# Kernel tuning notes

Measured on AMD Instinct MI355X. Metric: run time of the kernel, lower is better.

Reference implementation:

```python
import jax, jax.numpy as jnp
import numpy as np

NEG_SLOPE = 0.2  # PyG GATConv default negative_slope
EPS = 1e-16


def gat_conv(x, src, dst, num_nodes, W, att_src, att_dst, bias, concat):
    """PyG-style GATConv (eval mode, no dropout). att_*: [H, C]."""
    H, C = att_src.shape
    h = (x @ W).reshape(num_nodes, H, C)                      # [N,H,C]
    a_s = jnp.einsum('nhc,hc->nh', h, att_src)                # [N,H]
    a_d = jnp.einsum('nhc,hc->nh', h, att_dst)                # [N,H]
    e = jax.nn.leaky_relu(a_s[src] + a_d[dst], NEG_SLOPE)     # [E,H]
    # segment softmax over edges grouped by destination node
    m = jax.lax.stop_gradient(jax.ops.segment_max(e, dst, num_segments=num_nodes))
    ex = jnp.exp(e - m[dst])
    denom = jax.ops.segment_sum(ex, dst, num_segments=num_nodes)
    alpha = ex / (denom[dst] + EPS)                           # [E,H]
    msg = h[src] * alpha[:, :, None]                          # [E,H,C]
    out = jax.ops.segment_sum(msg, dst, num_segments=num_nodes)  # [N,H,C]
    out = out.reshape(num_nodes, H * C) if concat else out.mean(axis=1)
    return out + bias


def setup_inputs() -> dict:
    key = jax.random.key(0)
    ks = jax.random.split(key, 12)
    N, E = 65536, 1310720
    IN, HID, OUT, HEADS = 768, 128, 2, 8
    C1 = HID // HEADS  # 16
    s = 0.05
    return {
        'x': jax.random.normal(ks[0], (N, IN), jnp.float32),
        'edge_index': jax.random.randint(ks[1], (2, E), 0, N, jnp.int64),
        'W1': jax.random.normal(ks[2], (IN, HEADS * C1), jnp.float32) * s,
        'att_src1': jax.random.normal(ks[3], (HEADS, C1), jnp.float32) * s,
        'att_dst1': jax.random.normal(ks[4], (HEADS, C1), jnp.float32) * s,
        'b1': jnp.zeros((HID,), jnp.float32),
        'Wp': jax.random.normal(ks[5], (IN, HID), jnp.float32) * s,
        'bp': jnp.zeros((HID,), jnp.float32),
        'W2': jax.random.normal(ks[6], (HID, OUT), jnp.float32) * s,
        'att_src2': jax.random.normal(ks[7], (1, OUT), jnp.float32) * s,
        'att_dst2': jax.random.normal(ks[8], (1, OUT), jnp.float32) * s,
        'b2': jnp.zeros((OUT,), jnp.float32),
    }


def reference(x, edge_index, W1, att_src1, att_dst1, b1, Wp, bp, W2, att_src2, att_dst2, b2):
    N = x.shape[0]
    loops = jnp.arange(N, dtype=edge_index.dtype)  # add_self_loops=True
    src = jnp.concatenate([edge_index[0], loops])
    dst = jnp.concatenate([edge_index[1], loops])
    # eval mode: dropout is identity
    h1 = gat_conv(x, src, dst, N, W1, att_src1, att_dst1, b1, concat=True)
    h = jax.nn.elu(h1 + x @ Wp + bp)  # residual projection + ELU
    return gat_conv(h, src, dst, N, W2, att_src2, att_dst2, b2, concat=False)
```

## Files before the change

kernel.cpp:

```cpp
#include <hip/hip_runtime.h>
#include <hip/hip_bf16.h>
#include <math.h>

#define NEG_SLOPE 0.2f

typedef __attribute__((ext_vector_type(8))) short short8;
typedef __attribute__((ext_vector_type(4))) float float4v;

__device__ __forceinline__ unsigned f2bf(float f) {
  unsigned u = __builtin_bit_cast(unsigned, f);
  return (u + 0x7fffu + ((u >> 16) & 1u)) >> 16;
}
__device__ __forceinline__ float bflo(unsigned u) {
  return __builtin_bit_cast(float, u << 16);
}
__device__ __forceinline__ float bfhi(unsigned u) {
  return __builtin_bit_cast(float, u & 0xffff0000u);
}

__global__ __launch_bounds__(256) void convert_w(const float* __restrict__ W1,
                                                 const float* __restrict__ Wp,
                                                 short* __restrict__ Wt) {
  int k = blockIdx.x;
  int c = threadIdx.x;
  float v = (c < 128) ? W1[k * 128 + c] : Wp[k * 128 + (c - 128)];
  Wt[(size_t)c * 768 + k] = (short)f2bf(v);
}

__global__ __launch_bounds__(256) void gemm_mfma(const float* __restrict__ x,
                                                 const short* __restrict__ Wt,
                                                 float* __restrict__ proj,
                                                 unsigned* __restrict__ h1bf) {
  __shared__ short As[64][40];
  __shared__ short Bs[256][40];
  const int tid = threadIdx.x;
  const int wave = tid >> 6, lane = tid & 63;
  const int l15 = lane & 15, l4 = lane >> 4;
  const int row0 = blockIdx.x * 64;

  const int ar = tid >> 3;
  const int ak = (tid & 7) * 4;
  const int bc = tid >> 2;
  const int bk = (tid & 3) * 8;

  float4v acc[4][4] = {};

  for (int k0 = 0; k0 < 768; k0 += 32) {
#pragma unroll
    for (int i = 0; i < 2; i++) {
      int r = i * 32 + ar;
      float4 f = *(const float4*)&x[(size_t)(row0 + r) * 768 + k0 + ak];
      uint2 p;
      p.x = f2bf(f.x) | (f2bf(f.y) << 16);
      p.y = f2bf(f.z) | (f2bf(f.w) << 16);
      *(uint2*)&As[r][ak] = p;
    }
#pragma unroll
    for (int i = 0; i < 4; i++) {
      int c = i * 64 + bc;
      uint4 v = *(const uint4*)&Wt[(size_t)c * 768 + k0 + bk];
      *(uint4*)&Bs[c][bk] = v;
    }
    __syncthreads();

    short8 afr[4];
#pragma unroll
    for (int rt = 0; rt < 4; rt++)
      afr[rt] = *(const short8*)&As[rt * 16 + l15][l4 * 8];
#pragma unroll
    for (int ct = 0; ct < 4; ct++) {
      short8 bfr = *(const short8*)&Bs[wave * 64 + ct * 16 + l15][l4 * 8];
#pragma unroll
      for (int rt = 0; rt < 4; rt++)
        acc[rt][ct] =
            __builtin_amdgcn_mfma_f32_16x16x32_bf16(afr[rt], bfr, acc[rt][ct], 0, 0, 0);
    }
    __syncthreads();
  }

  const int colbase = wave * 64;
  if (wave < 2) {
#pragma unroll
    for (int ct = 0; ct < 4; ct++) {
      const int c = colbase + ct * 16 + l15;
#pragma unroll
      for (int rt = 0; rt < 4; rt++) {
#pragma unroll
        for (int r = 0; r < 4; r++) {
          const int R = row0 + rt * 16 + l4 * 4 + r;
          unsigned u = f2bf(acc[rt][ct][r]);
          unsigned up = __shfl_xor(u, 1);
          if ((l15 & 1) == 0) h1bf[(size_t)R * 64 + (c >> 1)] = u | (up << 16);
        }
      }
    }
  } else {
#pragma unroll
    for (int ct = 0; ct < 4; ct++) {
      const int c = colbase - 128 + ct * 16 + l15;
#pragma unroll
      for (int rt = 0; rt < 4; rt++) {
#pragma unroll
        for (int r = 0; r < 4; r++) {
          const int R = row0 + rt * 16 + l4 * 4 + r;
          proj[(size_t)R * 128 + c] = acc[rt][ct][r];
        }
      }
    }
  }
}

__global__ __launch_bounds__(256) void attn1b(const uint4* __restrict__ h1bf4,
                                              const float* __restrict__ att_src1,
                                              const float* __restrict__ att_dst1,
                                              float* __restrict__ a_s1,
                                              float* __restrict__ a_d1) {
  const int t = blockIdx.x * 256 + threadIdx.x;
  const int n = t >> 3, h = t & 7;
  uint4 q0 = h1bf4[(size_t)n * 16 + h * 2];
  uint4 q1 = h1bf4[(size_t)n * 16 + h * 2 + 1];
  float v[16];
  v[0] = bflo(q0.x); v[1] = bfhi(q0.x); v[2] = bflo(q0.y); v[3] = bfhi(q0.y);
  v[4] = bflo(q0.z); v[5] = bfhi(q0.z); v[6] = bflo(q0.w); v[7] = bfhi(q0.w);
  v[8] = bflo(q1.x); v[9] = bfhi(q1.x); v[10] = bflo(q1.y); v[11] = bfhi(q1.y);
  v[12] = bflo(q1.z); v[13] = bfhi(q1.z); v[14] = bflo(q1.w); v[15] = bfhi(q1.w);
  float as = 0.f, ad = 0.f;
#pragma unroll
  for (int i = 0; i < 16; i++) {
    as += v[i] * att_src1[h * 16 + i];
    ad += v[i] * att_dst1[h * 16 + i];
  }
  a_s1[t] = as;
  a_d1[t] = ad;
}

__global__ void init_counts(int* counts, int N) {
  int i = blockIdx.x * blockDim.x + threadIdx.x;
  if (i < N) counts[i] = 1;
}

__global__ void hist_kernel(const int* __restrict__ dst, int* counts, int E) {
  int i = blockIdx.x * blockDim.x + threadIdx.x;
  int base = i * 4;
  if (base + 3 < E) {
    int4 d = *(const int4*)&dst[base];
    atomicAdd(&counts[d.x], 1);
    atomicAdd(&counts[d.y], 1);
    atomicAdd(&counts[d.z], 1);
    atomicAdd(&counts[d.w], 1);
  } else {
    for (int j = base; j < E; j++) atomicAdd(&counts[dst[j]], 1);
  }
}

__global__ __launch_bounds__(256) void scan_a(const int* __restrict__ counts,
                                              int* offsets, int* bsum) {
  __shared__ int s[256];
  int t = threadIdx.x, idx = blockIdx.x * 256 + t;
  int v = counts[idx];
  s[t] = v;
  __syncthreads();
  for (int d = 1; d < 256; d <<= 1) {
    int x = (t >= d) ? s[t - d] : 0;
    __syncthreads();
    s[t] += x;
    __syncthreads();
  }
  offsets[idx] = s[t] - v;
  if (t == 255) bsum[blockIdx.x] = s[t];
}

__global__ __launch_bounds__(256) void scan_b(int* bsum) {
  __shared__ int s[256];
  int t = threadIdx.x;
  int v = bsum[t];
  s[t] = v;
  __syncthreads();
  for (int d = 1; d < 256; d <<= 1) {
    int x = (t >= d) ? s[t - d] : 0;
    __syncthreads();
    s[t] += x;
    __syncthreads();
  }
  bsum[t] = s[t] - v;
}

__global__ __launch_bounds__(256) void scan_c(int* offsets, const int* bsum,
                                              int* cursor, int* sortedsrc,
                                              int N, int Etot) {
  int t = threadIdx.x, idx = blockIdx.x * 256 + t;
  int off = offsets[idx] + bsum[blockIdx.x];
  offsets[idx] = off;
  sortedsrc[off] = idx;
  cursor[idx] = off + 1;
  if (idx == 0) offsets[N] = Etot;
}

__global__ void scatter_edges(const int* __restrict__ src,
                              const int* __restrict__ dst, int* cursor,
                              int* sortedsrc, int E) {
  int i = blockIdx.x * blockDim.x + threadIdx.x;
  int base = i * 4;
  if (base + 3 < E) {
    int4 s = *(const int4*)&src[base];
    int4 d = *(const int4*)&dst[base];
    sortedsrc[atomicAdd(&cursor[d.x], 1)] = s.x;
    sortedsrc[atomicAdd(&cursor[d.y], 1)] = s.y;
    sortedsrc[atomicAdd(&cursor[d.z], 1)] = s.z;
    sortedsrc[atomicAdd(&cursor[d.w], 1)] = s.w;
  } else {
    for (int j = base; j < E; j++)
      sortedsrc[atomicAdd(&cursor[dst[j]], 1)] = src[j];
  }
}

__global__ __launch_bounds__(256) void agg1_fused(
    const uint4* __restrict__ h1bf4, const float* __restrict__ proj,
    const float* __restrict__ a_s1, const float* __restrict__ a_d1,
    const int* __restrict__ offsets, const int* __restrict__ sortedsrc,
    const float* __restrict__ b1, const float* __restrict__ bp,
    const float* __restrict__ W2, const float* __restrict__ att_s2,
    const float* __restrict__ att_d2, float* __restrict__ h2,
    float* __restrict__ as2, float* __restrict__ ad2) {
  const int t = threadIdx.x;
  const int n = blockIdx.x * 16 + (t >> 4);
  const int k = t & 15;
  const int hd = k >> 1;
  const float ad = a_d1[n * 8 + hd];
  const int begin = offsets[n], end = offsets[n + 1];
  float acc[8] = {};
  float aw = 0.f;
  int j = begin;
  for (; j + 4 <= end; j += 4) {
    int s0 = sortedsrc[j], s1 = sortedsrc[j + 1];
    int s2 = sortedsrc[j + 2], s3 = sortedsrc[j + 3];
    float e0 = a_s1[s0 * 8 + hd], e1 = a_s1[s1 * 8 + hd];
    float e2 = a_s1[s2 * 8 + hd], e3 = a_s1[s3 * 8 + hd];
    uint4 q0 = h1bf4[(size_t)s0 * 16 + k];
    uint4 q1 = h1bf4[(size_t)s1 * 16 + k];
    uint4 q2 = h1bf4[(size_t)s2 * 16 + k];
    uint4 q3 = h1bf4[(size_t)s3 * 16 + k];
    e0 += ad; e1 += ad; e2 += ad; e3 += ad;
    float w0 = __expf(e0 > 0.f ? e0 : NEG_SLOPE * e0);
    float w1 = __expf(e1 > 0.f ? e1 : NEG_SLOPE * e1);
    float w2 = __expf(e2 > 0.f ? e2 : NEG_SLOPE * e2);
    float w3 = __expf(e3 > 0.f ? e3 : NEG_SLOPE * e3);
    acc[0] += w0 * bflo(q0.x) + w1 * bflo(q1.x) + w2 * bflo(q2.x) + w3 * bflo(q3.x);
    acc[1] += w0 * bfhi(q0.x) + w1 * bfhi(q1.x) + w2 * bfhi(q2.x) + w3 * bfhi(q3.x);
    acc[2] += w0 * bflo(q0.y) + w1 * bflo(q1.y) + w2 * bflo(q2.y) + w3 * bflo(q3.y);
    acc[3] += w0 * bfhi(q0.y) + w1 * bfhi(q1.y) + w2 * bfhi(q2.y) + w3 * bfhi(q3.y);
    acc[4] += w0 * bflo(q0.z) + w1 * bflo(q1.z) + w2 * bflo(q2.z) + w3 * bflo(q3.z);
    acc[5] += w0 * bfhi(q0.z) + w1 * bfhi(q1.z) + w2 * bfhi(q2.z) + w3 * bfhi(q3.z);
    acc[6] += w0 * bflo(q0.w) + w1 * bflo(q1.w) + w2 * bflo(q2.w) + w3 * bflo(q3.w);
    acc[7] += w0 * bfhi(q0.w) + w1 * bfhi(q1.w) + w2 * bfhi(q2.w) + w3 * bfhi(q3.w);
    aw += (w0 + w1) + (w2 + w3);
  }
  for (; j < end; j++) {
    int s0 = sortedsrc[j];
    float e0 = a_s1[s0 * 8 + hd] + ad;
    uint4 q0 = h1bf4[(size_t)s0 * 16 + k];
    float w0 = __expf(e0 > 0.f ? e0 : NEG_SLOPE * e0);
    acc[0] += w0 * bflo(q0.x);
    acc[1] += w0 * bfhi(q0.x);
    acc[2] += w0 * bflo(q0.y);
    acc[3] += w0 * bfhi(q0.y);
    acc[4] += w0 * bflo(q0.z);
    acc[5] += w0 * bfhi(q0.z);
    acc[6] += w0 * bflo(q0.w);
    acc[7] += w0 * bfhi(q0.w);
    aw += w0;
  }
  const float inv = 1.f / (aw + 1e-16f);
  const float4 pj0 = *(const float4*)&proj[(size_t)n * 128 + k * 8];
  const float4 pj1 = *(const float4*)&proj[(size_t)n * 128 + k * 8 + 4];
  const float4 b1a = *(const float4*)&b1[k * 8];
  const float4 b1b = *(const float4*)&b1[k * 8 + 4];
  const float4 bpa = *(const float4*)&bp[k * 8];
  const float4 bpb = *(const float4*)&bp[k * 8 + 4];
  float v[8];
  v[0] = acc[0] * inv + pj0.x + b1a.x + bpa.x;
  v[1] = acc[1] * inv + pj0.y + b1a.y + bpa.y;
  v[2] = acc[2] * inv + pj0.z + b1a.z + bpa.z;
  v[3] = acc[3] * inv + pj0.w + b1a.w + bpa.w;
  v[4] = acc[4] * inv + pj1.x + b1b.x + bpb.x;
  v[5] = acc[5] * inv + pj1.y + b1b.y + bpb.y;
  v[6] = acc[6] * inv + pj1.z + b1b.z + bpb.z;
  v[7] = acc[7] * inv + pj1.w + b1b.w + bpb.w;
  float p0 = 0.f, p1 = 0.f;
#pragma unroll
  for (int i = 0; i < 8; i++) {
    float vi = v[i] > 0.f ? v[i] : (__expf(v[i]) - 1.f);
    float2 w2 = *(const float2*)&W2[(k * 8 + i) * 2];
    p0 += vi * w2.x;
    p1 += vi * w2.y;
  }
#pragma unroll
  for (int off = 8; off; off >>= 1) {
    p0 += __shfl_xor(p0, off);
    p1 += __shfl_xor(p1, off);
  }
  if (k == 0) {
    h2[2 * n] = p0;
    h2[2 * n + 1] = p1;
    as2[n] = p0 * att_s2[0] + p1 * att_s2[1];
    ad2[n] = p0 * att_d2[0] + p1 * att_d2[1];
  }
}

__global__ __launch_bounds__(256) void agg2(
    const float* __restrict__ h2, const float* __restrict__ as2,
    const float* __restrict__ ad2, const int* __restrict__ offsets,
    const int* __restrict__ sortedsrc, const float* __restrict__ b2,
    float* __restrict__ out, int N) {
  const int node = blockIdx.x * 16 + (threadIdx.x >> 4);
  const int lane = threadIdx.x & 15;
  const int begin = offsets[node], end = offsets[node + 1];
  const float ad = ad2[node];
  float acc0 = 0.f, acc1 = 0.f, aw = 0.f;
  for (int j = begin + lane; j < end; j += 16) {
    int s = sortedsrc[j];
    float e = as2[s] + ad;
    float w = __expf(e > 0.f ? e : NEG_SLOPE * e);
    float2 hh = *(const float2*)&h2[2 * s];
    acc0 += w * hh.x;
    acc1 += w * hh.y;
    aw += w;
  }
#pragma unroll
  for (int off = 8; off; off >>= 1) {
    acc0 += __shfl_xor(acc0, off);
    acc1 += __shfl_xor(acc1, off);
    aw += __shfl_xor(aw, off);
  }
  if (lane == 0) {
    float inv = 1.f / (aw + 1e-16f);
    out[2 * node] = acc0 * inv + b2[0];
    out[2 * node + 1] = acc1 * inv + b2[1];
  }
}

extern "C" void kernel_launch(void* const* d_in, const int* in_sizes, int n_in,
                              void* d_out, int out_size, void* d_ws,
                              size_t ws_size, hipStream_t stream) {
  const float* x = (const float*)d_in[0];
  const int* edge_index = (const int*)d_in[1];
  const float* W1 = (const float*)d_in[2];
  const float* att_src1 = (const float*)d_in[3];
  const float* att_dst1 = (const float*)d_in[4];
  const float* b1 = (const float*)d_in[5];
  const float* Wp = (const float*)d_in[6];
  const float* bp = (const float*)d_in[7];
  const float* W2 = (const float*)d_in[8];
  const float* att_src2 = (const float*)d_in[9];
  const float* att_dst2 = (const float*)d_in[10];
  const float* b2 = (const float*)d_in[11];
  float* out = (float*)d_out;

  const int N = in_sizes[0] / 768;
  const int E = in_sizes[1] / 2;
  const int Etot = E + N;
  const int* src = edge_index;
  const int* dst = edge_index + E;

  char* ws = (char*)d_ws;
  size_t off = 0;
  auto alloc = [&](size_t bytes) {
    size_t cur = off;
    off += (bytes + 255) & ~(size_t)255;
    return (void*)(ws + cur);
  };
  float* proj = (float*)alloc((size_t)N * 128 * 4);
  unsigned* h1bf = (unsigned*)alloc((size_t)N * 64 * 4);
  float* a_s1 = (float*)alloc((size_t)N * 8 * 4);
  float* a_d1 = (float*)alloc((size_t)N * 8 * 4);
  float* h2 = (float*)alloc((size_t)N * 2 * 4);
  float* as2 = (float*)alloc((size_t)N * 4);
  float* ad2 = (float*)alloc((size_t)N * 4);
  int* counts = (int*)alloc((size_t)N * 4);
  int* offsets = (int*)alloc(((size_t)N + 1) * 4);
  int* cursor = (int*)alloc((size_t)N * 4);
  int* bsum = (int*)alloc(256 * 4);
  int* sortedsrc = (int*)alloc((size_t)Etot * 4);
  short* Wt = (short*)alloc((size_t)256 * 768 * 2);

  convert_w<<<768, 256, 0, stream>>>(W1, Wp, Wt);
  gemm_mfma<<<N / 64, 256, 0, stream>>>(x, Wt, proj, h1bf);
  attn1b<<<N * 8 / 256, 256, 0, stream>>>((const uint4*)h1bf, att_src1,
                                          att_dst1, a_s1, a_d1);
  init_counts<<<(N + 255) / 256, 256, 0, stream>>>(counts, N);
  hist_kernel<<<(E / 4 + 255) / 256, 256, 0, stream>>>(dst, counts, E);
  scan_a<<<N / 256, 256, 0, stream>>>(counts, offsets, bsum);
  scan_b<<<1, 256, 0, stream>>>(bsum);
  scan_c<<<N / 256, 256, 0, stream>>>(offsets, bsum, cursor, sortedsrc, N,
                                      Etot);
  scatter_edges<<<(E / 4 + 255) / 256, 256, 0, stream>>>(src, dst, cursor,
                                                         sortedsrc, E);
  agg1_fused<<<N / 16, 256, 0, stream>>>((const uint4*)h1bf, proj, a_s1, a_d1,
                                         offsets, sortedsrc, b1, bp, W2,
                                         att_src2, att_dst2, h2, as2, ad2);
  agg2<<<N / 16, 256, 0, stream>>>(h2, as2, ad2, offsets, sortedsrc, b2, out,
                                   N);
}
```

Measured before the change: 568.1 us.

## Drop LDS staging in GEMM, fuse small kernels, split agg1 edges across two half-groups

The GEMM now loads A and B fragments straight from global memory into registers, so there is no shared-memory staging and no __syncthreads. The count initialisation is folded into convert_w, and the block-sum scan is folded into scan_c, with each block redoing the 256-entry scan. agg1_fused now gives each node 32 lanes: two 16-lane halves work on interleaved groups of 4 edges, masked tail lanes replace the scalar remainder loop, and the halves are combined with a shuffle. Together these cut launch count and barrier overhead and add memory-level parallelism in the gather, but the GEMM loses LDS reuse, since each wave reloads x rows and each block re-reads Wt from cache.

Measured after the change: 624.9 us. 1.1x slower.

```diff
diff --git a/kernel.cpp b/kernel.cpp
--- a/kernel.cpp
+++ b/kernel.cpp
@@ -20,62 +20,59 @@
 
 __global__ __launch_bounds__(256) void convert_w(const float* __restrict__ W1,
                                                  const float* __restrict__ Wp,
-                                                 short* __restrict__ Wt) {
+                                                 short* __restrict__ Wt,
+                                                 int* __restrict__ counts,
+                                                 int N) {
   int k = blockIdx.x;
   int c = threadIdx.x;
   float v = (c < 128) ? W1[k * 128 + c] : Wp[k * 128 + (c - 128)];
   Wt[(size_t)c * 768 + k] = (short)f2bf(v);
+  int i = blockIdx.x * 256 + threadIdx.x;
+  if (i < N) counts[i] = 1;
 }
 
 __global__ __launch_bounds__(256) void gemm_mfma(const float* __restrict__ x,
                                                  const short* __restrict__ Wt,
                                                  float* __restrict__ proj,
                                                  unsigned* __restrict__ h1bf) {
-  __shared__ short As[64][40];
-  __shared__ short Bs[256][40];
   const int tid = threadIdx.x;
   const int wave = tid >> 6, lane = tid & 63;
   const int l15 = lane & 15, l4 = lane >> 4;
   const int row0 = blockIdx.x * 64;
 
-  const int ar = tid >> 3;
-  const int ak = (tid & 7) * 4;
-  const int bc = tid >> 2;
-  const int bk = (tid & 3) * 8;
+  const float* xrow[4];
+#pragma unroll
+  for (int rt = 0; rt < 4; rt++)
+    xrow[rt] = x + (size_t)(row0 + rt * 16 + l15) * 768 + l4 * 8;
+  const short* wcol[4];
+#pragma unroll
+  for (int ct = 0; ct < 4; ct++)
+    wcol[ct] = Wt + (size_t)(wave * 64 + ct * 16 + l15) * 768 + l4 * 8;
 
   float4v acc[4][4] = {};
 
+#pragma unroll 2
   for (int k0 = 0; k0 < 768; k0 += 32) {
-#pragma unroll
-    for (int i = 0; i < 2; i++) {
-      int r = i * 32 + ar;
-      float4 f = *(const float4*)&x[(size_t)(row0 + r) * 768 + k0 + ak];
-      uint2 p;
-      p.x = f2bf(f.x) | (f2bf(f.y) << 16);
-      p.y = f2bf(f.z) | (f2bf(f.w) << 16);
-      *(uint2*)&As[r][ak] = p;
+    short8 afr[4], bfr[4];
+#pragma unroll
+    for (int rt = 0; rt < 4; rt++) {
+      float4 fa = *(const float4*)(xrow[rt] + k0);
+      float4 fb = *(const float4*)(xrow[rt] + k0 + 4);
+      uint4 pk;
+      pk.x = f2bf(fa.x) | (f2bf(fa.y) << 16);
+      pk.y = f2bf(fa.z) | (f2bf(fa.w) << 16);
+      pk.z = f2bf(fb.x) | (f2bf(fb.y) << 16);
+      pk.w = f2bf(fb.z) | (f2bf(fb.w) << 16);
+      afr[rt] = __builtin_bit_cast(short8, pk);
     }
 #pragma unroll
-    for (int i = 0; i < 4; i++) {
-      int c = i * 64 + bc;
-      uint4 v = *(const uint4*)&Wt[(size_t)c * 768 + k0 + bk];
-      *(uint4*)&Bs[c][bk] = v;
-    }
-    __syncthreads();
-
-    short8 afr[4];
-#pragma unroll
-    for (int rt = 0; rt < 4; rt++)
-      afr[rt] = *(const short8*)&As[rt * 16 + l15][l4 * 8];
-#pragma unroll
-    for (int ct = 0; ct < 4; ct++) {
-      short8 bfr = *(const short8*)&Bs[wave * 64 + ct * 16 + l15][l4 * 8];
+    for (int ct = 0; ct < 4; ct++) bfr[ct] = *(const short8*)(wcol[ct] + k0);
+#pragma unroll
+    for (int ct = 0; ct < 4; ct++)
 #pragma unroll
       for (int rt = 0; rt < 4; rt++)
         acc[rt][ct] =
-            __builtin_amdgcn_mfma_f32_16x16x32_bf16(afr[rt], bfr, acc[rt][ct], 0, 0, 0);
-    }
-    __syncthreads();
+            __builtin_amdgcn_mfma_f32_16x16x32_bf16(afr[rt], bfr[ct], acc[rt][ct], 0, 0, 0);
   }
 
   const int colbase = wave * 64;
@@ -134,11 +131,6 @@
   a_d1[t] = ad;
 }
 
-__global__ void init_counts(int* counts, int N) {
-  int i = blockIdx.x * blockDim.x + threadIdx.x;
-  if (i < N) counts[i] = 1;
-}
-
 __global__ void hist_kernel(const int* __restrict__ dst, int* counts, int E) {
   int i = blockIdx.x * blockDim.x + threadIdx.x;
   int base = i * 4;
@@ -170,11 +162,13 @@
   if (t == 255) bsum[blockIdx.x] = s[t];
 }
 
-__global__ __launch_bounds__(256) void scan_b(int* bsum) {
+__global__ __launch_bounds__(256) void scan_c(int* offsets,
+                                              const int* __restrict__ bsum,
+                                              int* cursor, int* sortedsrc,
+                                              int N, int Etot) {
   __shared__ int s[256];
-  int t = threadIdx.x;
-  int v = bsum[t];
-  s[t] = v;
+  int t = threadIdx.x, idx = blockIdx.x * 256 + t;
+  s[t] = bsum[t];
   __syncthreads();
   for (int d = 1; d < 256; d <<= 1) {
     int x = (t >= d) ? s[t - d] : 0;
@@ -182,14 +176,8 @@
     s[t] += x;
     __syncthreads();
   }
-  bsum[t] = s[t] - v;
-}
-
-__global__ __launch_bounds__(256) void scan_c(int* offsets, const int* bsum,
-                                              int* cursor, int* sortedsrc,
-                                              int N, int Etot) {
-  int t = threadIdx.x, idx = blockIdx.x * 256 + t;
-  int off = offsets[idx] + bsum[blockIdx.x];
+  int blockpref = (blockIdx.x == 0) ? 0 : s[blockIdx.x - 1];
+  int off = offsets[idx] + blockpref;
   offsets[idx] = off;
   sortedsrc[off] = idx;
   cursor[idx] = off + 1;
@@ -223,17 +211,21 @@
     const float* __restrict__ att_d2, float* __restrict__ h2,
     float* __restrict__ as2, float* __restrict__ ad2) {
   const int t = threadIdx.x;
-  const int n = blockIdx.x * 16 + (t >> 4);
+  const int n = blockIdx.x * 8 + (t >> 5);
+  const int sub = (t >> 4) & 1;
   const int k = t & 15;
   const int hd = k >> 1;
   const float ad = a_d1[n * 8 + hd];
   const int begin = offsets[n], end = offsets[n + 1];
   float acc[8] = {};
   float aw = 0.f;
-  int j = begin;
-  for (; j + 4 <= end; j += 4) {
-    int s0 = sortedsrc[j], s1 = sortedsrc[j + 1];
-    int s2 = sortedsrc[j + 2], s3 = sortedsrc[j + 3];
+  for (int jj = begin + sub * 4; jj < end; jj += 8) {
+    const bool v0 = jj < end, v1 = jj + 1 < end, v2 = jj + 2 < end,
+               v3 = jj + 3 < end;
+    int s0 = sortedsrc[v0 ? jj : begin];
+    int s1 = sortedsrc[v1 ? jj + 1 : begin];
+    int s2 = sortedsrc[v2 ? jj + 2 : begin];
+    int s3 = sortedsrc[v3 ? jj + 3 : begin];
     float e0 = a_s1[s0 * 8 + hd], e1 = a_s1[s1 * 8 + hd];
     float e2 = a_s1[s2 * 8 + hd], e3 = a_s1[s3 * 8 + hd];
     uint4 q0 = h1bf4[(size_t)s0 * 16 + k];
@@ -241,10 +233,10 @@
     uint4 q2 = h1bf4[(size_t)s2 * 16 + k];
     uint4 q3 = h1bf4[(size_t)s3 * 16 + k];
     e0 += ad; e1 += ad; e2 += ad; e3 += ad;
-    float w0 = __expf(e0 > 0.f ? e0 : NEG_SLOPE * e0);
-    float w1 = __expf(e1 > 0.f ? e1 : NEG_SLOPE * e1);
-    float w2 = __expf(e2 > 0.f ? e2 : NEG_SLOPE * e2);
-    float w3 = __expf(e3 > 0.f ? e3 : NEG_SLOPE * e3);
+    float w0 = v0 ? __expf(e0 > 0.f ? e0 : NEG_SLOPE * e0) : 0.f;
+    float w1 = v1 ? __expf(e1 > 0.f ? e1 : NEG_SLOPE * e1) : 0.f;
+    float w2 = v2 ? __expf(e2 > 0.f ? e2 : NEG_SLOPE * e2) : 0.f;
+    float w3 = v3 ? __expf(e3 > 0.f ? e3 : NEG_SLOPE * e3) : 0.f;
     acc[0] += w0 * bflo(q0.x) + w1 * bflo(q1.x) + w2 * bflo(q2.x) + w3 * bflo(q3.x);
     acc[1] += w0 * bfhi(q0.x) + w1 * bfhi(q1.x) + w2 * bfhi(q2.x) + w3 * bfhi(q3.x);
     acc[2] += w0 * bflo(q0.y) + w1 * bflo(q1.y) + w2 * bflo(q2.y) + w3 * bflo(q3.y);
@@ -255,21 +247,10 @@
     acc[7] += w0 * bfhi(q0.w) + w1 * bfhi(q1.w) + w2 * bfhi(q2.w) + w3 * bfhi(q3.w);
     aw += (w0 + w1) + (w2 + w3);
   }
-  for (; j < end; j++) {
-    int s0 = sortedsrc[j];
-    float e0 = a_s1[s0 * 8 + hd] + ad;
-    uint4 q0 = h1bf4[(size_t)s0 * 16 + k];
-    float w0 = __expf(e0 > 0.f ? e0 : NEG_SLOPE * e0);
-    acc[0] += w0 * bflo(q0.x);
-    acc[1] += w0 * bfhi(q0.x);
-    acc[2] += w0 * bflo(q0.y);
-    acc[3] += w0 * bfhi(q0.y);
-    acc[4] += w0 * bflo(q0.z);
-    acc[5] += w0 * bfhi(q0.z);
-    acc[6] += w0 * bflo(q0.w);
-    acc[7] += w0 * bfhi(q0.w);
-    aw += w0;
-  }
+#pragma unroll
+  for (int i = 0; i < 8; i++) acc[i] += __shfl_xor(acc[i], 16);
+  aw += __shfl_xor(aw, 16);
+
   const float inv = 1.f / (aw + 1e-16f);
   const float4 pj0 = *(const float4*)&proj[(size_t)n * 128 + k * 8];
   const float4 pj1 = *(const float4*)&proj[(size_t)n * 128 + k * 8 + 4];
@@ -299,7 +280,7 @@
     p0 += __shfl_xor(p0, off);
     p1 += __shfl_xor(p1, off);
   }
-  if (k == 0) {
+  if ((t & 31) == 0) {
     h2[2 * n] = p0;
     h2[2 * n + 1] = p1;
     as2[n] = p0 * att_s2[0] + p1 * att_s2[1];
@@ -383,21 +364,19 @@
   int* sortedsrc = (int*)alloc((size_t)Etot * 4);
   short* Wt = (short*)alloc((size_t)256 * 768 * 2);
 
-  convert_w<<<768, 256, 0, stream>>>(W1, Wp, Wt);
+  convert_w<<<768, 256, 0, stream>>>(W1, Wp, Wt, counts, N);
   gemm_mfma<<<N / 64, 256, 0, stream>>>(x, Wt, proj, h1bf);
   attn1b<<<N * 8 / 256, 256, 0, stream>>>((const uint4*)h1bf, att_src1,
                                           att_dst1, a_s1, a_d1);
-  init_counts<<<(N + 255) / 256, 256, 0, stream>>>(counts, N);
   hist_kernel<<<(E / 4 + 255) / 256, 256, 0, stream>>>(dst, counts, E);
   scan_a<<<N / 256, 256, 0, stream>>>(counts, offsets, bsum);
-  scan_b<<<1, 256, 0, stream>>>(bsum);
   scan_c<<<N / 256, 256, 0, stream>>>(offsets, bsum, cursor, sortedsrc, N,
                                       Etot);
   scatter_edges<<<(E / 4 + 255) / 256, 256, 0, stream>>>(src, dst, cursor,
                                                          sortedsrc, E);
-  agg1_fused<<<N / 16, 256, 0, stream>>>((const uint4*)h1bf, proj, a_s1, a_d1,
-                                         offsets, sortedsrc, b1, bp, W2,
-                                         att_src2, att_dst2, h2, as2, ad2);
+  agg1_fused<<<N / 8, 256, 0, stream>>>((const uint4*)h1bf, proj, a_s1, a_d1,
+                                        offsets, sortedsrc, b1, bp, W2,
+                                        att_src2, att_dst2, h2, as2, ad2);
   agg2<<<N / 16, 256, 0, stream>>>(h2, as2, ad2, offsets, sortedsrc, b2, out,
                                    N);
 }
```
